# Optimization experiments

Hardware: AMD Instinct MI355X
Metric: run time of the kernel (lower is better)

## Reference

```python
import jax, jax.numpy as jnp
import numpy as np

DIM = 1024
NUM_HEADS = 16
HEAD_DIM = DIM // NUM_HEADS  # 64
LATENT = 128
Q_RANK = 256
B, S = 4, 2048


def setup_inputs() -> dict:
    key = jax.random.key(0)
    ks = jax.random.split(key, 12)
    w = lambda k, shape: jax.random.normal(k, shape, dtype=jnp.float32) * 0.02
    x = jax.random.normal(ks[0], (B, S, DIM), dtype=jnp.float32)
    mask = jnp.tril(jnp.ones((S, S), dtype=jnp.int32))[None, None, :, :]  # causal [1,1,S,S]
    return {
        "x": x,
        "mask": mask,
        "w_kvc": w(ks[1], (DIM, LATENT)),   "b_kvc": jnp.zeros((LATENT,), jnp.float32),
        "w_kvu": w(ks[2], (LATENT, 2 * DIM)), "b_kvu": jnp.zeros((2 * DIM,), jnp.float32),
        "w_qc":  w(ks[3], (DIM, Q_RANK)),   "b_qc": jnp.zeros((Q_RANK,), jnp.float32),
        "w_qu":  w(ks[4], (Q_RANK, DIM)),   "b_qu": jnp.zeros((DIM,), jnp.float32),
        "w_o":   w(ks[5], (DIM, DIM)),      "b_o": jnp.zeros((DIM,), jnp.float32),
    }


def reference(x, mask, w_kvc, b_kvc, w_kvu, b_kvu, w_qc, b_qc, w_qu, b_qu, w_o, b_o):
    b, s, _ = x.shape
    # low-rank KV path
    kv_latent = x @ w_kvc + b_kvc                      # [B,S,latent]
    kv_up = kv_latent @ w_kvu + b_kvu                  # [B,S,2*dim]
    K, V = jnp.split(kv_up, 2, axis=-1)                # each [B,S,dim]
    # low-rank Q path
    Q = (x @ w_qc + b_qc) @ w_qu + b_qu                # [B,S,dim]

    def split_heads(t):  # [B,S,dim] -> [B,H,S,hd]
        return t.reshape(b, s, NUM_HEADS, HEAD_DIM).transpose(0, 2, 1, 3)

    Qh, Kh, Vh = split_heads(Q), split_heads(K), split_heads(V)
    scores = jnp.einsum("bhsd,bhtd->bhst", Qh, Kh) / np.sqrt(HEAD_DIM).astype(np.float32)
    scores = jnp.where(mask == 0, jnp.float32(-1e9), scores)
    attn = jax.nn.softmax(scores, axis=-1)
    ctx = jnp.einsum("bhst,bhtd->bhsd", attn, Vh)      # [B,H,S,hd]
    ctx = ctx.transpose(0, 2, 1, 3).reshape(b, s, DIM)
    return ctx @ w_o + b_o
```

## Files before the change

kernel.cpp:

```cpp
#include <hip/hip_runtime.h>

typedef __attribute__((ext_vector_type(8))) short short8;
typedef __attribute__((ext_vector_type(4))) float f32x4;

#define DIM 1024
#define NH 16
#define HD 64
#define LAT 128
#define QR 256
#define NCAT (LAT + QR)
#define BB 4
#define SS 2048
#define BS (BB * SS)

#define SCALE_LOG2E 0.18033688011112042f

__device__ __forceinline__ unsigned short f2b(float f) {
  unsigned int u = __builtin_bit_cast(unsigned int, f);
  u += 0x7FFFu + ((u >> 16) & 1u);
  return (unsigned short)(u >> 16);
}
__device__ __forceinline__ float b2f(unsigned short h) {
  unsigned int u = ((unsigned int)h) << 16;
  return __builtin_bit_cast(float, u);
}
__device__ __forceinline__ unsigned int pack_bf16_pair(float f0, float f1) {
  unsigned int u0 = __builtin_bit_cast(unsigned int, f0) + 0x8000u;
  unsigned int u1 = __builtin_bit_cast(unsigned int, f1) + 0x8000u;
  return __builtin_amdgcn_perm(u1, u0, 0x07060302u);
}
__device__ __forceinline__ void gll16(const unsigned short* g, unsigned short* l) {
  __builtin_amdgcn_global_load_lds(
      (const __attribute__((address_space(1))) unsigned int*)g,
      (__attribute__((address_space(3))) unsigned int*)l, 16, 0, 0);
}

__global__ __launch_bounds__(256) void cvt_x(const float* __restrict__ in,
                                             unsigned short* __restrict__ out, int n4) {
  int i = blockIdx.x * 256 + threadIdx.x;
  if (i >= n4) return;
  f32x4 v = ((const f32x4*)in)[i];
  ushort4 o;
  o.x = f2b(v[0]); o.y = f2b(v[1]); o.z = f2b(v[2]); o.w = f2b(v[3]);
  ((ushort4*)out)[i] = o;
}

__global__ __launch_bounds__(256) void prep_weights(
    const float* __restrict__ w_kvc, const float* __restrict__ w_qc,
    const float* __restrict__ w_kvu, const float* __restrict__ w_qu,
    const float* __restrict__ w_o, const float* __restrict__ b_kvc,
    const float* __restrict__ b_qc, unsigned short* __restrict__ wcatT,
    unsigned short* __restrict__ wkvuT, unsigned short* __restrict__ wquT,
    unsigned short* __restrict__ woT, float* __restrict__ bias_cat) {
  __shared__ unsigned short T[64 * 72];
  const int id = blockIdx.x;
  const int tid = threadIdx.x;
  if (id >= 480) {
    if (tid < LAT) bias_cat[tid] = b_kvc[tid];
    else bias_cat[tid] = b_qc[tid - LAT];
    if (tid < 128) bias_cat[tid + 256] = b_qc[tid + 128];
    return;
  }
  const float* in; unsigned short* out; int K, N, tile;
  if (id < 32)       { in = w_kvc; out = wcatT;                       K = DIM; N = LAT;     tile = id; }
  else if (id < 96)  { in = w_qc;  out = wcatT + (size_t)LAT * DIM;   K = DIM; N = QR;      tile = id - 32; }
  else if (id < 160) { in = w_kvu; out = wkvuT;                       K = LAT; N = 2 * DIM; tile = id - 96; }
  else if (id < 224) { in = w_qu;  out = wquT;                        K = QR;  N = DIM;     tile = id - 160; }
  else               { in = w_o;   out = woT;                         K = DIM; N = DIM;     tile = id - 224; }
  const int ktiles = K >> 6;
  const int k0 = (tile % ktiles) * 64, n0 = (tile / ktiles) * 64;
  {
    const int r = tid >> 2, cq = (tid & 3) * 16;
#pragma unroll
    for (int j = 0; j < 4; ++j) {
      f32x4 v = *(const f32x4*)(in + (size_t)(k0 + r) * N + n0 + cq + j * 4);
      ushort4 o;
      o.x = f2b(v[0]); o.y = f2b(v[1]); o.z = f2b(v[2]); o.w = f2b(v[3]);
      *(ushort4*)(T + r * 72 + cq + j * 4) = o;
    }
  }
  __syncthreads();
#pragma unroll
  for (int s = 0; s < 2; ++s) {
    int idx = tid + s * 256;
    int nr = idx >> 3, kg = (idx & 7) * 8;
    short8 o;
#pragma unroll
    for (int i = 0; i < 8; i++) o[i] = T[(kg + i) * 72 + nr];
    *(short8*)(out + (size_t)(n0 + nr) * K + k0 + kg) = o;
  }
}

__global__ __launch_bounds__(256, 4) void gemm_lds(const unsigned short* __restrict__ A,
                                                   const unsigned short* __restrict__ WT,
                                                   const float* __restrict__ bias,
                                                   float* __restrict__ outF,
                                                   unsigned short* __restrict__ outB,
                                                   unsigned short* __restrict__ vtOut,
                                                   int N, int K, int lda, int ldout,
                                                   float scale, int nblk) {
  __shared__ unsigned short gsm[17408];
  unsigned short* As = gsm;
  unsigned short* Bs = gsm + 8192;
  const int tid = threadIdx.x;
  const int wave = tid >> 6, lane = tid & 63;
  const int ln = lane & 15, quad = lane >> 4;
  const int chunk = nblk >> 3;
  const int sw = (blockIdx.x & 7) * chunk + (blockIdx.x >> 3);
  const int nwx = N >> 7;
  const int bx = sw % nwx, by = sw / nwx;
  const int m0 = by * 128, n0 = bx * 128;
  const int wm = (wave >> 1) * 64, wn = (wave & 1) * 64;

  const int srow = wave * 32 + (lane >> 3);
  const int scol = (lane & 7) * 8;
  const unsigned short* Ag = A + (size_t)(m0 + srow) * lda + scol;
  const unsigned short* Bg = WT + (size_t)(n0 + srow) * K + scol;
  unsigned short* Al = As + wave * 32 * 64;
  unsigned short* Bl = Bs + wave * 32 * 64;

  f32x4 acc[4][4];
#pragma unroll
  for (int i = 0; i < 4; i++)
#pragma unroll
    for (int j = 0; j < 4; j++) acc[i][j] = (f32x4){0.f, 0.f, 0.f, 0.f};

  for (int k0 = 0; k0 < K; k0 += 64) {
    __syncthreads();
#pragma unroll
    for (int i = 0; i < 4; i++) {
      gll16(Ag + (size_t)i * 8 * lda + k0, Al + i * 8 * 64);
      gll16(Bg + (size_t)i * 8 * K + k0, Bl + i * 8 * 64);
    }
    __syncthreads();
#pragma unroll
    for (int kc = 0; kc < 2; kc++) {
      short8 af[4], bf[4];
#pragma unroll
      for (int i = 0; i < 4; i++) {
        af[i] = *(const short8*)(As + (wm + i * 16 + ln) * 64 + kc * 32 + quad * 8);
        bf[i] = *(const short8*)(Bs + (wn + i * 16 + ln) * 64 + kc * 32 + quad * 8);
      }
#pragma unroll
      for (int mi = 0; mi < 4; mi++)
#pragma unroll
        for (int ni = 0; ni < 4; ni++)
          acc[mi][ni] =
              __builtin_amdgcn_mfma_f32_16x16x32_bf16(af[mi], bf[ni], acc[mi][ni], 0, 0, 0);
    }
  }

  if (vtOut && n0 >= DIM) {
    __syncthreads();
#pragma unroll
    for (int mi = 0; mi < 4; mi++) {
      const int s = wm + mi * 16 + quad * 4;
#pragma unroll
      for (int ni = 0; ni < 4; ni++) {
        const int d = wn + ni * 16 + ln;
        const float bv = bias[n0 + d];
#pragma unroll
        for (int r = 0; r < 4; r++)
          gsm[d * 136 + s + r] = f2b(acc[mi][ni][r] + bv);
      }
    }
    __syncthreads();
    const int d0 = n0 - DIM, bb = m0 >> 11, s0l = m0 & (SS - 1);
#pragma unroll
    for (int t = 0; t < 8; ++t) {
      int idx = tid + t * 256;
      int dr = idx >> 4, cs = (idx & 15) * 8;
      short8 v = *(const short8*)(gsm + dr * 136 + cs);
      *(short8*)(vtOut + (size_t)(bb * DIM + d0 + dr) * SS + s0l + cs) = v;
    }
    return;
  }

#pragma unroll
  for (int mi = 0; mi < 4; mi++) {
    const int row = m0 + wm + mi * 16 + quad * 4;
#pragma unroll
    for (int ni = 0; ni < 4; ni++) {
      const int col = n0 + wn + ni * 16 + ln;
      const float bv = bias[col];
#pragma unroll
      for (int r = 0; r < 4; r++) {
        float v = (acc[mi][ni][r] + bv) * scale;
        size_t o = (size_t)(row + r) * ldout + col;
        if (outF) outF[o] = v;
        if (outB) outB[o] = f2b(v);
      }
    }
  }
}

__global__ __launch_bounds__(256, 4) void attn_mfma(const unsigned short* __restrict__ Qb,
                                                    const unsigned short* __restrict__ KVb,
                                                    const unsigned short* __restrict__ VTb,
                                                    unsigned short* __restrict__ ctxB) {
  __shared__ unsigned short smem[12288];
  unsigned short* Ks = smem;
  unsigned short* Vts = smem + 4096;
  unsigned short* Ps = smem + 8192;
  const int tid = threadIdx.x;
  const int wave = tid >> 6, lane = tid & 63;
  const int ln = lane & 15, quad = lane >> 4;
  const int hw = blockIdx.x;
  const int xcd = hw & 7, slot = hw >> 3;
  const int grp = xcd * 8 + (slot >> 4);
  const int pair = slot & 15;
  const int h = grp & 15, b = grp >> 4;
  const int tA = pair, tB = 31 - pair;
  const int s0A = tA * 64, s0B = tB * 64;
  const int ktmaxB = tB;
  const int qminA = s0A + wave * 16, qmaxA = qminA + 15;
  const int qminB = s0B + wave * 16, qmaxB = qminB + 15;

  short8 qfA[2], qfB[2];
  {
    const unsigned short* qa =
        Qb + (size_t)(b * SS + s0A + wave * 16 + ln) * DIM + h * HD + quad * 8;
    qfA[0] = *(const short8*)qa;
    qfA[1] = *(const short8*)(qa + 32);
    const unsigned short* qb2 =
        Qb + (size_t)(b * SS + s0B + wave * 16 + ln) * DIM + h * HD + quad * 8;
    qfB[0] = *(const short8*)qb2;
    qfB[1] = *(const short8*)(qb2 + 32);
  }

  f32x4 ocA[4], ocB[4];
  float lpA = 0.f, lpB = 0.f;
#pragma unroll
  for (int i = 0; i < 4; i++) {
    ocA[i] = (f32x4){0.f, 0.f, 0.f, 0.f};
    ocB[i] = (f32x4){0.f, 0.f, 0.f, 0.f};
  }

  unsigned short* Pw = Ps + wave * (16 * 64);
  const int swz = (ln & 7) << 3;

  const int srow = tid >> 3, sc8 = (tid & 7) * 8;
  const int ssc = sc8 ^ ((srow & 7) << 3);

  const unsigned short* kptr =
      KVb + (size_t)(b * SS + srow) * (2 * DIM) + h * HD + sc8;
  const unsigned short* vptr = VTb + (size_t)(b * DIM + h * HD + srow) * SS + sc8;
  const size_t kstep = (size_t)64 * 2 * DIM;
  const size_t krow32 = (size_t)32 * 2 * DIM;
  const size_t vrow32 = (size_t)32 * SS;

  short8 kreg0 = *(const short8*)kptr;
  short8 kreg1 = *(const short8*)(kptr + krow32);
  short8 vreg0 = *(const short8*)vptr;
  short8 vreg1 = *(const short8*)(vptr + vrow32);

  for (int kt = 0; kt <= ktmaxB; ++kt) {
    __syncthreads();
    *(short8*)(Ks + srow * 64 + ssc) = kreg0;
    *(short8*)(Ks + (srow + 32) * 64 + ssc) = kreg1;
    *(short8*)(Vts + srow * 64 + ssc) = vreg0;
    *(short8*)(Vts + (srow + 32) * 64 + ssc) = vreg1;
    __syncthreads();
    if (kt < ktmaxB) {
      kptr += kstep; vptr += 64;
      kreg0 = *(const short8*)kptr;
      kreg1 = *(const short8*)(kptr + krow32);
      vreg0 = *(const short8*)vptr;
      vreg1 = *(const short8*)(vptr + vrow32);
    }

    const int k0g = kt * 64;

    auto stream = [&](const short8* qf, f32x4* oc, float& lp, const int qminw,
                      const int qmaxw) {
      if (k0g > qmaxw) return;
      const bool needmask = (k0g + 63 > qminw);

      f32x4 sacc[4];
#pragma unroll
      for (int nt = 0; nt < 4; nt++) sacc[nt] = (f32x4){0.f, 0.f, 0.f, 0.f};
      __builtin_amdgcn_s_setprio(1);
#pragma unroll
      for (int kc = 0; kc < 2; kc++) {
        const int rc = (kc * 32 + quad * 8) ^ swz;
#pragma unroll
        for (int nt = 0; nt < 4; nt++) {
          if (k0g + nt * 16 > qmaxw) continue;
          short8 kfrag = *(const short8*)(Ks + (nt * 16 + ln) * 64 + rc);
          sacc[nt] =
              __builtin_amdgcn_mfma_f32_16x16x32_bf16(kfrag, qf[kc], sacc[nt], 0, 0, 0);
        }
      }
      __builtin_amdgcn_s_setprio(0);

      const int qg = qminw + ln;
      float lt = 0.f;
      if (!needmask) {
#pragma unroll
        for (int nt = 0; nt < 4; nt++) {
          float p0 = __builtin_exp2f(sacc[nt][0]);
          float p1 = __builtin_exp2f(sacc[nt][1]);
          float p2 = __builtin_exp2f(sacc[nt][2]);
          float p3 = __builtin_exp2f(sacc[nt][3]);
          uint2 pw;
          pw.x = pack_bf16_pair(p0, p1);
          pw.y = pack_bf16_pair(p2, p3);
          *(uint2*)(Pw + ln * 64 + ((nt * 16 + quad * 4) ^ swz)) = pw;
          lt += (p0 + p1) + (p2 + p3);
        }
      } else {
#pragma unroll
        for (int nt = 0; nt < 4; nt++) {
          const int base = k0g + nt * 16 + quad * 4;
          float pe[4];
#pragma unroll
          for (int r = 0; r < 4; r++) {
            float p = __builtin_exp2f(sacc[nt][r]);
            if (base + r > qg) p = 0.f;
            pe[r] = p;
          }
          uint2 pw;
          pw.x = pack_bf16_pair(pe[0], pe[1]);
          pw.y = pack_bf16_pair(pe[2], pe[3]);
          *(uint2*)(Pw + ln * 64 + ((nt * 16 + quad * 4) ^ swz)) = pw;
          lt += (pe[0] + pe[1]) + (pe[2] + pe[3]);
        }
      }
      lp += lt;

      __builtin_amdgcn_s_setprio(1);
#pragma unroll
      for (int kc = 0; kc < 2; kc++) {
        if (k0g + kc * 32 > qmaxw) continue;
        const int rc = (kc * 32 + quad * 8) ^ swz;
        short8 pfrag = *(const short8*)(Pw + ln * 64 + rc);
#pragma unroll
        for (int dt = 0; dt < 4; dt++) {
          short8 vfrag = *(const short8*)(Vts + (dt * 16 + ln) * 64 + rc);
          oc[dt] =
              __builtin_amdgcn_mfma_f32_16x16x32_bf16(pfrag, vfrag, oc[dt], 0, 0, 0);
        }
      }
      __builtin_amdgcn_s_setprio(0);
    };

    stream(qfA, ocA, lpA, qminA, qmaxA);
    stream(qfB, ocB, lpB, qminB, qmaxB);
  }

  lpA += __shfl_xor(lpA, 16, 64);
  lpA += __shfl_xor(lpA, 32, 64);
  lpB += __shfl_xor(lpB, 16, 64);
  lpB += __shfl_xor(lpB, 32, 64);
  float liA[4], liB[4];
#pragma unroll
  for (int r = 0; r < 4; r++) {
    liA[r] = 1.f / __shfl(lpA, quad * 4 + r, 64);
    liB[r] = 1.f / __shfl(lpB, quad * 4 + r, 64);
  }

  __syncthreads();
#pragma unroll
  for (int r = 0; r < 4; r++) {
#pragma unroll
    for (int dt = 0; dt < 4; dt++)
      smem[(wave * 16 + quad * 4 + r) * 72 + dt * 16 + ln] = f2b(ocA[dt][r] * liA[r]);
  }
  __syncthreads();
#pragma unroll
  for (int t = 0; t < 2; ++t) {
    int idx = tid + t * 256;
    int row = idx >> 3, c = idx & 7;
    short8 v = *(const short8*)(smem + row * 72 + c * 8);
    *(short8*)(ctxB + (size_t)(b * SS + s0A + row) * DIM + h * HD + c * 8) = v;
  }
  __syncthreads();
#pragma unroll
  for (int r = 0; r < 4; r++) {
#pragma unroll
    for (int dt = 0; dt < 4; dt++)
      smem[(wave * 16 + quad * 4 + r) * 72 + dt * 16 + ln] = f2b(ocB[dt][r] * liB[r]);
  }
  __syncthreads();
#pragma unroll
  for (int t = 0; t < 2; ++t) {
    int idx = tid + t * 256;
    int row = idx >> 3, c = idx & 7;
    short8 v = *(const short8*)(smem + row * 72 + c * 8);
    *(short8*)(ctxB + (size_t)(b * SS + s0B + row) * DIM + h * HD + c * 8) = v;
  }
}

extern "C" void kernel_launch(void* const* d_in, const int* in_sizes, int n_in,
                              void* d_out, int out_size, void* d_ws, size_t ws_size,
                              hipStream_t stream) {
  const float* x     = (const float*)d_in[0];
  const float* w_kvc = (const float*)d_in[2];
  const float* b_kvc = (const float*)d_in[3];
  const float* w_kvu = (const float*)d_in[4];
  const float* b_kvu = (const float*)d_in[5];
  const float* w_qc  = (const float*)d_in[6];
  const float* b_qc  = (const float*)d_in[7];
  const float* w_qu  = (const float*)d_in[8];
  const float* b_qu  = (const float*)d_in[9];
  const float* w_o   = (const float*)d_in[10];
  const float* b_o   = (const float*)d_in[11];
  float* out = (float*)d_out;

  unsigned short* xb     = (unsigned short*)d_ws;
  unsigned short* wcatT  = xb + (size_t)BS * DIM;
  unsigned short* wkvuT  = wcatT + (size_t)NCAT * DIM;
  unsigned short* wquT   = wkvuT + (size_t)LAT * 2 * DIM;
  unsigned short* woT    = wquT + (size_t)QR * DIM;
  unsigned short* kvqlat = woT + (size_t)DIM * DIM;
  unsigned short* kvup   = kvqlat + (size_t)BS * NCAT;
  unsigned short* Qbuf   = kvup + (size_t)BS * 2 * DIM;
  unsigned short* ctx    = Qbuf + (size_t)BS * DIM;
  float* bias_cat        = (float*)(ctx + (size_t)BS * DIM);

  cvt_x<<<(BS * DIM / 4 + 255) / 256, 256, 0, stream>>>(x, xb, BS * DIM / 4);
  prep_weights<<<481, 256, 0, stream>>>(w_kvc, w_qc, w_kvu, w_qu, w_o, b_kvc, b_qc,
                                        wcatT, wkvuT, wquT, woT, bias_cat);

  gemm_lds<<<dim3(BS / 128 * (NCAT / 128)), 256, 0, stream>>>(
      xb, wcatT, bias_cat, nullptr, kvqlat, nullptr, NCAT, DIM, DIM, NCAT, 1.0f,
      BS / 128 * (NCAT / 128));
  unsigned short* VT = xb;
  gemm_lds<<<dim3(BS / 128 * (2 * DIM / 128)), 256, 0, stream>>>(
      kvqlat, wkvuT, b_kvu, nullptr, kvup, VT, 2 * DIM, LAT, NCAT, 2 * DIM, 1.0f,
      BS / 128 * (2 * DIM / 128));
  gemm_lds<<<dim3(BS / 128 * (DIM / 128)), 256, 0, stream>>>(
      kvqlat + LAT, wquT, b_qu, nullptr, Qbuf, nullptr, DIM, QR, NCAT, DIM, SCALE_LOG2E,
      BS / 128 * (DIM / 128));
  attn_mfma<<<dim3(32 * NH * BB / 2), 256, 0, stream>>>(Qbuf, kvup, VT, ctx);
  gemm_lds<<<dim3(BS / 128 * (DIM / 128)), 256, 0, stream>>>(
      ctx, woT, b_o, out, nullptr, nullptr, DIM, DIM, DIM, DIM, 1.0f,
      BS / 128 * (DIM / 128));
}
```

Before: 267.0 us.

## Double-buffer GEMM LDS tiles with 32-wide K steps to overlap loads

Restructures the GEMM main loop to use two LDS buffers of 32-wide K slices, issuing the next slice's global-to-LDS loads before computing on the current one. This leaves one barrier per iteration instead of two, and global load latency can overlap with MFMA work. In exchange there are twice as many iterations, each doing half the MFMAs, and correctness depends on the async loads being complete by the following barrier.

New measurement: 254.8 us. 1.05x faster.

```diff
diff --git a/kernel.cpp b/kernel.cpp
--- a/kernel.cpp
+++ b/kernel.cpp
@@ -100,8 +100,6 @@
                                                    int N, int K, int lda, int ldout,
                                                    float scale, int nblk) {
   __shared__ unsigned short gsm[17408];
-  unsigned short* As = gsm;
-  unsigned short* Bs = gsm + 8192;
   const int tid = threadIdx.x;
   const int wave = tid >> 6, lane = tid & 63;
   const int ln = lane & 15, quad = lane >> 4;
@@ -112,12 +110,10 @@
   const int m0 = by * 128, n0 = bx * 128;
   const int wm = (wave >> 1) * 64, wn = (wave & 1) * 64;
 
-  const int srow = wave * 32 + (lane >> 3);
-  const int scol = (lane & 7) * 8;
+  const int srow = wave * 32 + (lane >> 2);
+  const int scol = (lane & 3) * 8;
   const unsigned short* Ag = A + (size_t)(m0 + srow) * lda + scol;
   const unsigned short* Bg = WT + (size_t)(n0 + srow) * K + scol;
-  unsigned short* Al = As + wave * 32 * 64;
-  unsigned short* Bl = Bs + wave * 32 * 64;
 
   f32x4 acc[4][4];
 #pragma unroll
@@ -125,33 +121,42 @@
 #pragma unroll
     for (int j = 0; j < 4; j++) acc[i][j] = (f32x4){0.f, 0.f, 0.f, 0.f};
 
-  for (int k0 = 0; k0 < K; k0 += 64) {
+#define STAGE(buf, kk)                                                        \
+  {                                                                           \
+    unsigned short* Al = gsm + (buf) * 4096 + wave * 1024;                    \
+    unsigned short* Bl = gsm + 8192 + (buf) * 4096 + wave * 1024;             \
+    gll16(Ag + (kk), Al);                                                     \
+    gll16(Ag + (size_t)16 * lda + (kk), Al + 512);                            \
+    gll16(Bg + (kk), Bl);                                                     \
+    gll16(Bg + (size_t)16 * K + (kk), Bl + 512);                              \
+  }
+
+  STAGE(0, 0);
+  __syncthreads();
+  const int T = K >> 5;
+  int cur = 0;
+  for (int t = 0; t < T; ++t) {
+    if (t + 1 < T) STAGE(cur ^ 1, (t + 1) * 32);
+    const unsigned short* Ab = gsm + cur * 4096;
+    const unsigned short* Bb = gsm + 8192 + cur * 4096;
+    short8 af[4], bf[4];
+#pragma unroll
+    for (int i = 0; i < 4; i++) {
+      af[i] = *(const short8*)(Ab + (wm + i * 16 + ln) * 32 + quad * 8);
+      bf[i] = *(const short8*)(Bb + (wn + i * 16 + ln) * 32 + quad * 8);
+    }
+#pragma unroll
+    for (int mi = 0; mi < 4; mi++)
+#pragma unroll
+      for (int ni = 0; ni < 4; ni++)
+        acc[mi][ni] =
+            __builtin_amdgcn_mfma_f32_16x16x32_bf16(af[mi], bf[ni], acc[mi][ni], 0, 0, 0);
     __syncthreads();
-#pragma unroll
-    for (int i = 0; i < 4; i++) {
-      gll16(Ag + (size_t)i * 8 * lda + k0, Al + i * 8 * 64);
-      gll16(Bg + (size_t)i * 8 * K + k0, Bl + i * 8 * 64);
-    }
-    __syncthreads();
-#pragma unroll
-    for (int kc = 0; kc < 2; kc++) {
-      short8 af[4], bf[4];
-#pragma unroll
-      for (int i = 0; i < 4; i++) {
-        af[i] = *(const short8*)(As + (wm + i * 16 + ln) * 64 + kc * 32 + quad * 8);
-        bf[i] = *(const short8*)(Bs + (wn + i * 16 + ln) * 64 + kc * 32 + quad * 8);
-      }
-#pragma unroll
-      for (int mi = 0; mi < 4; mi++)
-#pragma unroll
-        for (int ni = 0; ni < 4; ni++)
-          acc[mi][ni] =
-              __builtin_amdgcn_mfma_f32_16x16x32_bf16(af[mi], bf[ni], acc[mi][ni], 0, 0, 0);
-    }
-  }
+    cur ^= 1;
+  }
+#undef STAGE
 
   if (vtOut && n0 >= DIM) {
-    __syncthreads();
 #pragma unroll
     for (int mi = 0; mi < 4; mi++) {
       const int s = wm + mi * 16 + quad * 4;
```
